# Kernel tuning notes

Hardware: AMD Instinct MI355X
Metric: run time of the kernel (lower is better)

Reference implementation:

```python
import jax, jax.numpy as jnp
import numpy as np

N, E, D = 10000, 160000, 512
H, C = 4, 128          # hidden layers: 4 heads x 128 = 512 (residual-compatible)
HF, CF = 2, 512        # final layer: 2 heads, concat=False (mean)
NEG_SLOPE = 0.2


def _gat(x, src, dst, W, a_src, a_dst, b, heads, out_c, concat):
    """PyG-style GATConv (v1 attention), no dropout (eval mode)."""
    n = x.shape[0]
    h = (x @ W).reshape(n, heads, out_c)                  # [N,H,C]
    es = (h * a_src).sum(-1)                              # [N,H]
    ed = (h * a_dst).sum(-1)                              # [N,H]
    e = jax.nn.leaky_relu(es[src] + ed[dst], NEG_SLOPE)   # [E,H]
    m = jax.ops.segment_max(e, dst, num_segments=n)       # softmax over in-edges of dst
    m = jnp.where(jnp.isfinite(m), m, 0.0)                # guard isolated nodes
    ex = jnp.exp(e - m[dst])
    den = jax.ops.segment_sum(ex, dst, num_segments=n)
    alpha = ex / (den[dst] + 1e-16)                       # [E,H]
    msg = h[src] * alpha[..., None]                       # [E,H,C]
    out = jax.ops.segment_sum(msg, dst, num_segments=n)   # [N,H,C]
    out = out.reshape(n, heads * out_c) if concat else out.mean(axis=1)
    return out + b


def setup_inputs() -> dict:
    key = jax.random.key(0)
    ks = jax.random.split(key, 16)
    s = 0.05
    return {
        "graph": jax.random.normal(ks[0], (N, D), jnp.float32),
        "edge_index": jax.random.randint(ks[1], (2, E), 0, N, dtype=jnp.int32),
        "W1": jax.random.normal(ks[2], (D, H * C), jnp.float32) * s,
        "as1": jax.random.normal(ks[3], (H, C), jnp.float32) * s,
        "ad1": jax.random.normal(ks[4], (H, C), jnp.float32) * s,
        "b1": jnp.zeros((H * C,), jnp.float32),
        "W2": jax.random.normal(ks[5], (H * C, H * C), jnp.float32) * s,
        "as2": jax.random.normal(ks[6], (H, C), jnp.float32) * s,
        "ad2": jax.random.normal(ks[7], (H, C), jnp.float32) * s,
        "b2": jnp.zeros((H * C,), jnp.float32),
        "W3": jax.random.normal(ks[8], (H * C, HF * CF), jnp.float32) * s,
        "as3": jax.random.normal(ks[9], (HF, CF), jnp.float32) * s,
        "ad3": jax.random.normal(ks[10], (HF, CF), jnp.float32) * s,
        "b3": jnp.zeros((CF,), jnp.float32),
    }


def reference(graph, edge_index, W1, as1, ad1, b1, W2, as2, ad2, b2, W3, as3, ad3, b3):
    src, dst = edge_index[0], edge_index[1]
    # layer_size=2: conv1 + convs[0] with ELU+residual, convs[1] (concat=False) residual only
    x = jax.nn.elu(_gat(graph, src, dst, W1, as1, ad1, b1, H, C, True) + graph)
    x = jax.nn.elu(_gat(x, src, dst, W2, as2, ad2, b2, H, C, True) + x)
    x = _gat(x, src, dst, W3, as3, ad3, b3, HF, CF, False) + x
    return x
```

## Files before the change

### kernel.cpp

```cpp
#include <hip/hip_runtime.h>
#include <hip/hip_bf16.h>
#include <hip/hip_fp16.h>
#include <cstddef>
#include <cstdint>


typedef _Float16 half8 __attribute__((ext_vector_type(8)));
typedef _Float16 half4v __attribute__((ext_vector_type(4)));
typedef float floatx4 __attribute__((ext_vector_type(4)));

#define AS1(p) ((const __attribute__((address_space(1))) void*)(p))
#define AS3(p) ((__attribute__((address_space(3))) void*)(p))


__global__ void count_deg(const int* __restrict__ dst, int* __restrict__ deg, int E) {
    int e = blockIdx.x * blockDim.x + threadIdx.x;
    if (e < E) atomicAdd(&deg[dst[e]], 1);
}

__global__ void scan_kernel(const int* __restrict__ deg, int* __restrict__ row_start,
                            int* __restrict__ cursor, int n) {
    __shared__ int wsum[16];
    __shared__ int carry_s;
    int tid = threadIdx.x;
    int wave = tid >> 6, lane = tid & 63;
    if (tid == 0) { carry_s = 0; row_start[0] = 0; }
    __syncthreads();
    for (int base = 0; base < n; base += 1024) {
        int i = base + tid;
        int v = (i < n) ? deg[i] : 0;
        int x = v;
#pragma unroll
        for (int off = 1; off < 64; off <<= 1) {
            int t = __shfl_up(x, off);
            if (lane >= off) x += t;
        }
        if (lane == 63) wsum[wave] = x;
        __syncthreads();
        if (wave == 0 && lane < 16) {
            int w = wsum[lane];
#pragma unroll
            for (int off = 1; off < 16; off <<= 1) {
                int t = __shfl_up(w, off);
                if (lane >= off) w += t;
            }
            wsum[lane] = w;
        }
        __syncthreads();
        int carry = carry_s;
        int incl = x + (wave ? wsum[wave - 1] : 0) + carry;
        if (i < n) { row_start[i + 1] = incl; cursor[i] = incl - v; }
        __syncthreads();
        if (tid == 1023) carry_s = incl;
        __syncthreads();
    }
}

__global__ void scatter_edges(const int* __restrict__ src, const int* __restrict__ dst,
                              int* __restrict__ cursor, int* __restrict__ srcs, int E) {
    int e = blockIdx.x * blockDim.x + threadIdx.x;
    if (e < E) {
        int p = atomicAdd(&cursor[dst[e]], 1);
        srcs[p] = src[e];
    }
}


__global__ void cast_f16(const float* __restrict__ in, _Float16* __restrict__ out, int n4) {
    int i = blockIdx.x * blockDim.x + threadIdx.x;
    if (i < n4) {
        float4 v = ((const float4*)in)[i];
        half4v o = {(_Float16)v.x, (_Float16)v.y, (_Float16)v.z, (_Float16)v.w};
        ((half4v*)out)[i] = o;
    }
}

__global__ void prep_weights(const float* __restrict__ W1, const float* __restrict__ W2,
                             const float* __restrict__ W3,
                             _Float16* __restrict__ Wt1, _Float16* __restrict__ Wt2,
                             _Float16* __restrict__ Bt3) {
    __shared__ float t[32][33];
    int b = blockIdx.x;
    int region = b >> 8, idx = b & 255;
    int r0 = (idx >> 4) * 32, c0 = (idx & 15) * 32;
    const float* in;
    _Float16* out;
    int in_ld, out_ld;
    if (region == 0)      { in = W1;       out = Wt1;       in_ld = 512;  out_ld = 512;  }
    else if (region == 1) { in = W2;       out = Wt2;       in_ld = 512;  out_ld = 512;  }
    else if (region == 2) { in = W3;       out = Bt3;       in_ld = 1024; out_ld = 1024; }
    else                  { in = W3 + 512; out = Bt3 + 512; in_ld = 1024; out_ld = 1024; }
    int tx = threadIdx.x, ty = threadIdx.y;
    for (int i = ty; i < 32; i += 8)
        t[i][tx] = in[(size_t)(r0 + i) * in_ld + c0 + tx];
    __syncthreads();
    for (int i = ty; i < 32; i += 8)
        out[(size_t)(c0 + i) * out_ld + r0 + tx] = (_Float16)t[tx][i];
}

__global__ void proj_all(const float* __restrict__ W1, const float* __restrict__ as1,
                         const float* __restrict__ ad1,
                         const float* __restrict__ W2, const float* __restrict__ as2,
                         const float* __restrict__ ad2,
                         const float* __restrict__ W3, const float* __restrict__ as3,
                         const float* __restrict__ ad3,
                         _Float16* __restrict__ Wt1, _Float16* __restrict__ Wt2,
                         float* __restrict__ wes3, float* __restrict__ wed3) {
    int w = (blockIdx.x * blockDim.x + threadIdx.x) >> 6;
    int lane = threadIdx.x & 63;
    if (w < 8192) {
        int layer = w >> 12;
        int idx = w & 4095;
        int d = idx & 511, hh = (idx >> 9) & 3, sel = idx >> 11;
        const float* W = layer ? W2 : W1;
        const float* a = layer ? (sel ? ad2 : as2) : (sel ? ad1 : as1);
        const float* row = W + (size_t)d * 512 + hh * 128;
        const float* av = a + hh * 128;
        float s = 0.f;
        s += row[lane] * av[lane];
        s += row[lane + 64] * av[lane + 64];
#pragma unroll
        for (int off = 32; off; off >>= 1) s += __shfl_down(s, off);
        if (lane == 0) {
            _Float16* Wt = layer ? Wt2 : Wt1;
            Wt[(size_t)(512 + sel * 4 + hh) * 512 + d] = (_Float16)s;
        }
    } else if (w < 10240) {
        int idx = w - 8192;
        int k = idx & 511, hh = (idx >> 9) & 1, sel = idx >> 10;
        const float* a = (sel ? ad3 : as3) + hh * 512;
        const float* row = W3 + (size_t)k * 1024 + hh * 512;
        float s = 0.f;
        for (int c = lane; c < 512; c += 64) s += row[c] * a[c];
#pragma unroll
        for (int off = 32; off; off >>= 1) s += __shfl_down(s, off);
        if (lane == 0) (sel ? wed3 : wes3)[hh * 512 + k] = s;
    } else if (w < 11136) {
        int z = (w - 10240) * 64 + lane;
        int layer = z / 28672;
        int rem = z - layer * 28672;
        int row = 520 + rem / 512, col = rem & 511;
        (layer ? Wt2 : Wt1)[(size_t)row * 512 + col] = (_Float16)0.f;
    }
}


#define BK 64

__global__ __launch_bounds__(256) void gemm_f16_att(const _Float16* __restrict__ A,
                                                    const _Float16* __restrict__ Bt,
                                                    _Float16* __restrict__ Hout,
                                                    float* __restrict__ es,
                                                    float* __restrict__ ed,
                                                    int M, int K) {
    __shared__ _Float16 As[64 * BK];
    __shared__ _Float16 Bs[64 * BK];
    int tid = threadIdx.x;
    int lane = tid & 63, wave = tid >> 6;
    int wm = (wave & 1) * 32, wn = (wave >> 1) * 32;
    int m0 = blockIdx.y * 64, n0 = blockIdx.x * 64;
    int l15 = lane & 15, quad = lane >> 4;
    int trow = tid >> 3, tcol = tid & 7;

    floatx4 acc[2][2];
#pragma unroll
    for (int i = 0; i < 2; ++i)
#pragma unroll
        for (int j = 0; j < 2; ++j) acc[i][j] = (floatx4){0.f, 0.f, 0.f, 0.f};

    for (int k0 = 0; k0 < K; k0 += BK) {
        __syncthreads();
#pragma unroll
        for (int i = 0; i < 2; ++i) {
            int gr = m0 + i * 32 + trow; if (gr >= M) gr = M - 1;
            __builtin_amdgcn_global_load_lds(AS1(A + (size_t)gr * K + k0 + tcol * 8),
                                             AS3(As + (size_t)(i * 256 + tid) * 8), 16, 0, 0);
        }
#pragma unroll
        for (int i = 0; i < 2; ++i) {
            int gr = n0 + i * 32 + trow;
            __builtin_amdgcn_global_load_lds(AS1(Bt + (size_t)gr * K + k0 + tcol * 8),
                                             AS3(Bs + (size_t)(i * 256 + tid) * 8), 16, 0, 0);
        }
        __syncthreads();
#pragma unroll
        for (int ks = 0; ks < BK; ks += 32) {
            half8 af[2], bfr[2];
#pragma unroll
            for (int i = 0; i < 2; ++i)
                af[i] = *(const half8*)&As[(wm + i * 16 + l15) * BK + ks + quad * 8];
#pragma unroll
            for (int j = 0; j < 2; ++j)
                bfr[j] = *(const half8*)&Bs[(wn + j * 16 + l15) * BK + ks + quad * 8];
#pragma unroll
            for (int i = 0; i < 2; ++i)
#pragma unroll
                for (int j = 0; j < 2; ++j)
                    acc[i][j] = __builtin_amdgcn_mfma_f32_16x16x32_f16(af[i], bfr[j], acc[i][j], 0, 0, 0);
        }
    }
#pragma unroll
    for (int i = 0; i < 2; ++i)
#pragma unroll
        for (int j = 0; j < 2; ++j) {
            int col = n0 + wn + j * 16 + l15;
#pragma unroll
            for (int r = 0; r < 4; ++r) {
                int row = m0 + wm + i * 16 + quad * 4 + r;
                if (row < M) {
                    float v = acc[i][j][r];
                    if (col < 512) Hout[(size_t)row * 512 + col] = (_Float16)v;
                    else if (col < 516) es[row * 4 + col - 512] = v;
                    else if (col < 520) ed[row * 4 + col - 516] = v;
                }
            }
        }
}

__global__ __launch_bounds__(256) void gemm_f16_ep(const _Float16* __restrict__ A,
                                                   const _Float16* __restrict__ Bt,
                                                   float* __restrict__ out,
                                                   const float* __restrict__ bias,
                                                   const _Float16* __restrict__ xres,
                                                   int M, int Nn, int K) {
    __shared__ _Float16 As[64 * BK];
    __shared__ _Float16 Bs[64 * BK];
    int tid = threadIdx.x;
    int lane = tid & 63, wave = tid >> 6;
    int wm = (wave & 1) * 32, wn = (wave >> 1) * 32;
    int m0 = blockIdx.y * 64, n0 = blockIdx.x * 64;
    int l15 = lane & 15, quad = lane >> 4;
    int trow = tid >> 3, tcol = tid & 7;

    floatx4 acc[2][2];
#pragma unroll
    for (int i = 0; i < 2; ++i)
#pragma unroll
        for (int j = 0; j < 2; ++j) acc[i][j] = (floatx4){0.f, 0.f, 0.f, 0.f};

    for (int k0 = 0; k0 < K; k0 += BK) {
        __syncthreads();
#pragma unroll
        for (int i = 0; i < 2; ++i) {
            int gr = m0 + i * 32 + trow; if (gr >= M) gr = M - 1;
            __builtin_amdgcn_global_load_lds(AS1(A + (size_t)gr * K + k0 + tcol * 8),
                                             AS3(As + (size_t)(i * 256 + tid) * 8), 16, 0, 0);
        }
#pragma unroll
        for (int i = 0; i < 2; ++i) {
            int gr = n0 + i * 32 + trow;
            __builtin_amdgcn_global_load_lds(AS1(Bt + (size_t)gr * K + k0 + tcol * 8),
                                             AS3(Bs + (size_t)(i * 256 + tid) * 8), 16, 0, 0);
        }
        __syncthreads();
#pragma unroll
        for (int ks = 0; ks < BK; ks += 32) {
            half8 af[2], bfr[2];
#pragma unroll
            for (int i = 0; i < 2; ++i)
                af[i] = *(const half8*)&As[(wm + i * 16 + l15) * BK + ks + quad * 8];
#pragma unroll
            for (int j = 0; j < 2; ++j)
                bfr[j] = *(const half8*)&Bs[(wn + j * 16 + l15) * BK + ks + quad * 8];
#pragma unroll
            for (int i = 0; i < 2; ++i)
#pragma unroll
                for (int j = 0; j < 2; ++j)
                    acc[i][j] = __builtin_amdgcn_mfma_f32_16x16x32_f16(af[i], bfr[j], acc[i][j], 0, 0, 0);
        }
    }
#pragma unroll
    for (int i = 0; i < 2; ++i)
#pragma unroll
        for (int j = 0; j < 2; ++j) {
            int col = n0 + wn + j * 16 + l15;
#pragma unroll
            for (int r = 0; r < 4; ++r) {
                int row = m0 + wm + i * 16 + quad * 4 + r;
                if (row < M)
                    out[(size_t)row * Nn + col] =
                        0.5f * acc[i][j][r] + bias[col] + (float)xres[(size_t)row * Nn + col];
            }
        }
}


template <int H>
__global__ __launch_bounds__(256) void attn_alpha1(
    const float* __restrict__ es, const float* __restrict__ ed,
    const int* __restrict__ row_start, const int* __restrict__ srcs,
    float* __restrict__ alpha, float* __restrict__ den, int Nn, int E) {
    const int EP = 64 / H;
    int wave = threadIdx.x >> 6, lane = threadIdx.x & 63;
    int n = blockIdx.x * 4 + wave;
    if (n >= Nn) return;
    int h = lane & (H - 1);
    int eslot = lane / H;
    float edn = ed[n * H + h];
    int beg = row_start[n], end = row_start[n + 1];
    float dsum = 0.f;
    for (int j0 = beg; j0 < end; j0 += EP) {
        int j = j0 + eslot;
        if (j < end) {
            float e = es[srcs[j] * H + h] + edn;
            e = (e > 0.f) ? e : 0.2f * e;
            float w = __expf(e);
            alpha[(size_t)h * E + j] = w;
            dsum += w;
        }
    }
#pragma unroll
    for (int off = H; off < 64; off <<= 1) dsum += __shfl_xor(dsum, off);
    if (lane < H) den[n * H + lane] = dsum;
}


template <bool RES32, bool COEF3>
__global__ __launch_bounds__(512) void aggregate6_concat(
    const _Float16* __restrict__ h, const float* __restrict__ alpha,
    const float* __restrict__ den,
    const int* __restrict__ row_start, const int* __restrict__ srcs,
    const float* __restrict__ bias, const float* __restrict__ xres32,
    const _Float16* __restrict__ xres16, _Float16* __restrict__ x_out_h,
    const float* __restrict__ wes3, const float* __restrict__ wed3,
    float* __restrict__ es3, float* __restrict__ ed3, int Nn, int E) {
    int wave = threadIdx.x >> 6, lane = threadIdx.x & 63;
    int n = blockIdx.x * 8 + wave;
    if (n >= Nn) return;
    int head = lane >> 4;
    int c0 = lane * 8;
    const float* al = alpha + (size_t)head * E;
    int beg = row_start[n], end = row_start[n + 1];
    float acc[8] = {};
    int j = beg;
    for (; j + 3 < end; j += 4) {
        int s0 = srcs[j], s1 = srcs[j + 1], s2 = srcs[j + 2], s3 = srcs[j + 3];
        float w0 = al[j], w1 = al[j + 1], w2 = al[j + 2], w3 = al[j + 3];
        half8 h0 = *(const half8*)&h[(size_t)s0 * 512 + c0];
        half8 h1 = *(const half8*)&h[(size_t)s1 * 512 + c0];
        half8 h2 = *(const half8*)&h[(size_t)s2 * 512 + c0];
        half8 h3 = *(const half8*)&h[(size_t)s3 * 512 + c0];
#pragma unroll
        for (int k = 0; k < 8; ++k) acc[k] += w0 * (float)h0[k];
#pragma unroll
        for (int k = 0; k < 8; ++k) acc[k] += w1 * (float)h1[k];
#pragma unroll
        for (int k = 0; k < 8; ++k) acc[k] += w2 * (float)h2[k];
#pragma unroll
        for (int k = 0; k < 8; ++k) acc[k] += w3 * (float)h3[k];
    }
    for (; j < end; ++j) {
        int s = srcs[j];
        float w = al[j];
        half8 hv = *(const half8*)&h[(size_t)s * 512 + c0];
#pragma unroll
        for (int k = 0; k < 8; ++k) acc[k] += w * (float)hv[k];
    }
    float invden = 1.f / (den[n * 4 + head] + 1e-16f);
    size_t base = (size_t)n * 512 + c0;
    float v[8];
    half8 o;
#pragma unroll
    for (int k = 0; k < 8; ++k) {
        float res = RES32 ? xres32[base + k] : (float)xres16[base + k];
        float t = acc[k] * invden + bias[c0 + k] + res;
        t = (t > 0.f) ? t : expm1f(t);
        v[k] = t;
        o[k] = (_Float16)t;
    }
    *(half8*)&x_out_h[base] = o;
    if (COEF3) {
        float t0 = 0.f, t1 = 0.f, t2 = 0.f, t3 = 0.f;
#pragma unroll
        for (int k = 0; k < 8; ++k) {
            t0 += v[k] * wes3[c0 + k];
            t1 += v[k] * wes3[512 + c0 + k];
            t2 += v[k] * wed3[c0 + k];
            t3 += v[k] * wed3[512 + c0 + k];
        }
#pragma unroll
        for (int off = 32; off; off >>= 1) {
            t0 += __shfl_down(t0, off);
            t1 += __shfl_down(t1, off);
            t2 += __shfl_down(t2, off);
            t3 += __shfl_down(t3, off);
        }
        if (lane == 0) {
            es3[n * 2] = t0; es3[n * 2 + 1] = t1;
            ed3[n * 2] = t2; ed3[n * 2 + 1] = t3;
        }
    }
}


__global__ __launch_bounds__(512) void aggregate6_dual(
    const _Float16* __restrict__ x, const float* __restrict__ alpha,
    const float* __restrict__ den,
    const int* __restrict__ row_start, const int* __restrict__ srcs,
    _Float16* __restrict__ y, int Nn, int E) {
    int wave = threadIdx.x >> 6, lane = threadIdx.x & 63;
    int n = blockIdx.x * 8 + wave;
    if (n >= Nn) return;
    int c0 = lane * 8;
    const float* al0 = alpha;
    const float* al1 = alpha + E;
    int beg = row_start[n], end = row_start[n + 1];
    float a0[8] = {}, a1[8] = {};
    int j = beg;
    for (; j + 3 < end; j += 4) {
        int s0 = srcs[j], s1 = srcs[j + 1], s2 = srcs[j + 2], s3 = srcs[j + 3];
        float u0 = al0[j], u1 = al0[j + 1], u2 = al0[j + 2], u3 = al0[j + 3];
        float v0 = al1[j], v1 = al1[j + 1], v2 = al1[j + 2], v3 = al1[j + 3];
        half8 h0 = *(const half8*)&x[(size_t)s0 * 512 + c0];
        half8 h1 = *(const half8*)&x[(size_t)s1 * 512 + c0];
        half8 h2 = *(const half8*)&x[(size_t)s2 * 512 + c0];
        half8 h3 = *(const half8*)&x[(size_t)s3 * 512 + c0];
#pragma unroll
        for (int k = 0; k < 8; ++k) { float f = (float)h0[k]; a0[k] += u0 * f; a1[k] += v0 * f; }
#pragma unroll
        for (int k = 0; k < 8; ++k) { float f = (float)h1[k]; a0[k] += u1 * f; a1[k] += v1 * f; }
#pragma unroll
        for (int k = 0; k < 8; ++k) { float f = (float)h2[k]; a0[k] += u2 * f; a1[k] += v2 * f; }
#pragma unroll
        for (int k = 0; k < 8; ++k) { float f = (float)h3[k]; a0[k] += u3 * f; a1[k] += v3 * f; }
    }
    for (; j < end; ++j) {
        int s = srcs[j];
        float u = al0[j], v = al1[j];
        half8 hv = *(const half8*)&x[(size_t)s * 512 + c0];
#pragma unroll
        for (int k = 0; k < 8; ++k) { float f = (float)hv[k]; a0[k] += u * f; a1[k] += v * f; }
    }
    float invd0 = 1.f / (den[n * 2] + 1e-16f);
    float invd1 = 1.f / (den[n * 2 + 1] + 1e-16f);
    half8 o0, o1;
#pragma unroll
    for (int k = 0; k < 8; ++k) {
        o0[k] = (_Float16)(a0[k] * invd0);
        o1[k] = (_Float16)(a1[k] * invd1);
    }
    *(half8*)&y[(size_t)n * 1024 + c0] = o0;
    *(half8*)&y[(size_t)n * 1024 + 512 + c0] = o1;
}


extern "C" void kernel_launch(void* const* d_in, const int* in_sizes, int n_in,
                              void* d_out, int out_size, void* d_ws, size_t ws_size,
                              hipStream_t stream) {
    const float* graph = (const float*)d_in[0];
    const int* edge_index = (const int*)d_in[1];
    const float* W1 = (const float*)d_in[2];
    const float* as1 = (const float*)d_in[3];
    const float* ad1 = (const float*)d_in[4];
    const float* b1 = (const float*)d_in[5];
    const float* W2 = (const float*)d_in[6];
    const float* as2 = (const float*)d_in[7];
    const float* ad2 = (const float*)d_in[8];
    const float* b2 = (const float*)d_in[9];
    const float* W3 = (const float*)d_in[10];
    const float* as3 = (const float*)d_in[11];
    const float* ad3 = (const float*)d_in[12];
    const float* b3 = (const float*)d_in[13];

    const int D = 512;
    int N = in_sizes[0] / D;
    int E = in_sizes[1] / 2;
    const int* src = edge_index;
    const int* dst = edge_index + E;

    char* p = (char*)d_ws;
    auto carve = [&](size_t bytes) {
        void* r = (void*)p;
        p += (bytes + 255) & ~(size_t)255;
        return r;
    };
    _Float16* Ah   = (_Float16*)carve((size_t)N * 512 * 2);
    _Float16* Wt1  = (_Float16*)carve((size_t)576 * 512 * 2);
    _Float16* Wt2  = (_Float16*)carve((size_t)576 * 512 * 2);
    _Float16* Bt3  = (_Float16*)carve((size_t)512 * 1024 * 2);
    _Float16* h_h  = (_Float16*)carve((size_t)N * 1024 * 2);
    float* es      = (float*)carve((size_t)N * 4 * 4);
    float* ed      = (float*)carve((size_t)N * 4 * 4);
    float* den     = (float*)carve((size_t)N * 4 * 4);
    float* alpha   = (float*)carve((size_t)4 * E * 4);
    float* wes3    = (float*)carve((size_t)2 * 512 * 4);
    float* wed3    = (float*)carve((size_t)2 * 512 * 4);
    int* deg       = (int*)carve((size_t)N * 4);
    int* cur       = (int*)carve((size_t)N * 4);
    int* row_st    = (int*)carve((size_t)(N + 1) * 4);
    int* srcs      = (int*)carve((size_t)E * 4);

    hipMemsetAsync(deg, 0, (size_t)N * 4, stream);
    count_deg<<<(E + 255) / 256, 256, 0, stream>>>(dst, deg, E);
    scan_kernel<<<1, 1024, 0, stream>>>(deg, row_st, cur, N);
    scatter_edges<<<(E + 255) / 256, 256, 0, stream>>>(src, dst, cur, srcs, E);

    cast_f16<<<(N * 512 / 4 + 255) / 256, 256, 0, stream>>>(graph, Ah, N * 512 / 4);
    prep_weights<<<1024, dim3(32, 8), 0, stream>>>(W1, W2, W3, Wt1, Wt2, Bt3);
    proj_all<<<2784, 256, 0, stream>>>(W1, as1, ad1, W2, as2, ad2, W3, as3, ad3,
                                       Wt1, Wt2, wes3, wed3);

    int nblk4 = (N + 3) / 4;
    int nblk8 = (N + 7) / 8;
    int mblk = (N + 63) / 64;
    gemm_f16_att<<<dim3(9, mblk), 256, 0, stream>>>(Ah, Wt1, h_h, es, ed, N, 512);
    attn_alpha1<4><<<nblk4, 256, 0, stream>>>(es, ed, row_st, srcs, alpha, den, N, E);
    aggregate6_concat<true, false><<<nblk8, 512, 0, stream>>>(
        h_h, alpha, den, row_st, srcs, b1, graph, nullptr, Ah,
        nullptr, nullptr, nullptr, nullptr, N, E);

    gemm_f16_att<<<dim3(9, mblk), 256, 0, stream>>>(Ah, Wt2, h_h, es, ed, N, 512);
    attn_alpha1<4><<<nblk4, 256, 0, stream>>>(es, ed, row_st, srcs, alpha, den, N, E);
    aggregate6_concat<false, true><<<nblk8, 512, 0, stream>>>(
        h_h, alpha, den, row_st, srcs, b2, nullptr, Ah, Ah,
        wes3, wed3, es, ed, N, E);

    attn_alpha1<2><<<nblk4, 256, 0, stream>>>(es, ed, row_st, srcs, alpha, den, N, E);
    aggregate6_dual<<<nblk8, 512, 0, stream>>>(Ah, alpha, den, row_st, srcs, h_h, N, E);
    gemm_f16_ep<<<dim3(8, mblk), 256, 0, stream>>>(
        h_h, Bt3, (float*)d_out, b3, Ah, N, 512, 1024);
}
```

Baseline: 323.2 us.

## Fuse attention softmax weight computation into aggregation kernels

Drops the separate attn_alpha1 kernels and the alpha/den buffers, and computes the exp(leaky_relu(es[src]+ed[dst])) edge weights and their per-node sums inside the aggregation loops. This removes three kernel launches and the round trip of writing and re-reading a 4*E alpha array. In exchange, each lane recomputes its head's edge weight (redundant exp across the 16 lanes sharing a head) and does an extra gather of es per edge. Layer-3 coefficients now go to separate es3/ed3 buffers instead of overwriting es/ed.

```diff
diff --git a/kernel.cpp b/kernel.cpp
--- a/kernel.cpp
+++ b/kernel.cpp
@@ -11,6 +11,11 @@
 
 #define AS1(p) ((const __attribute__((address_space(1))) void*)(p))
 #define AS3(p) ((__attribute__((address_space(3))) void*)(p))
+
+__device__ __forceinline__ float leaky_exp(float e) {
+    e = (e > 0.f) ? e : 0.2f * e;
+    return __expf(e);
+}
 
 
 __global__ void count_deg(const int* __restrict__ dst, int* __restrict__ deg, int E) {
@@ -285,61 +290,36 @@
 }
 
 
-template <int H>
-__global__ __launch_bounds__(256) void attn_alpha1(
-    const float* __restrict__ es, const float* __restrict__ ed,
-    const int* __restrict__ row_start, const int* __restrict__ srcs,
-    float* __restrict__ alpha, float* __restrict__ den, int Nn, int E) {
-    const int EP = 64 / H;
-    int wave = threadIdx.x >> 6, lane = threadIdx.x & 63;
-    int n = blockIdx.x * 4 + wave;
-    if (n >= Nn) return;
-    int h = lane & (H - 1);
-    int eslot = lane / H;
-    float edn = ed[n * H + h];
-    int beg = row_start[n], end = row_start[n + 1];
-    float dsum = 0.f;
-    for (int j0 = beg; j0 < end; j0 += EP) {
-        int j = j0 + eslot;
-        if (j < end) {
-            float e = es[srcs[j] * H + h] + edn;
-            e = (e > 0.f) ? e : 0.2f * e;
-            float w = __expf(e);
-            alpha[(size_t)h * E + j] = w;
-            dsum += w;
-        }
-    }
-#pragma unroll
-    for (int off = H; off < 64; off <<= 1) dsum += __shfl_xor(dsum, off);
-    if (lane < H) den[n * H + lane] = dsum;
-}
-
-
 template <bool RES32, bool COEF3>
-__global__ __launch_bounds__(512) void aggregate6_concat(
-    const _Float16* __restrict__ h, const float* __restrict__ alpha,
-    const float* __restrict__ den,
+__global__ __launch_bounds__(512) void aggregate7_concat(
+    const _Float16* __restrict__ h, const float* __restrict__ es,
+    const float* __restrict__ ed,
     const int* __restrict__ row_start, const int* __restrict__ srcs,
     const float* __restrict__ bias, const float* __restrict__ xres32,
     const _Float16* __restrict__ xres16, _Float16* __restrict__ x_out_h,
     const float* __restrict__ wes3, const float* __restrict__ wed3,
-    float* __restrict__ es3, float* __restrict__ ed3, int Nn, int E) {
+    float* __restrict__ es3, float* __restrict__ ed3, int Nn) {
     int wave = threadIdx.x >> 6, lane = threadIdx.x & 63;
     int n = blockIdx.x * 8 + wave;
     if (n >= Nn) return;
     int head = lane >> 4;
     int c0 = lane * 8;
-    const float* al = alpha + (size_t)head * E;
+    float edn = ed[n * 4 + head];
     int beg = row_start[n], end = row_start[n + 1];
     float acc[8] = {};
+    float den = 0.f;
     int j = beg;
     for (; j + 3 < end; j += 4) {
         int s0 = srcs[j], s1 = srcs[j + 1], s2 = srcs[j + 2], s3 = srcs[j + 3];
-        float w0 = al[j], w1 = al[j + 1], w2 = al[j + 2], w3 = al[j + 3];
+        float e0 = es[s0 * 4 + head], e1 = es[s1 * 4 + head];
+        float e2 = es[s2 * 4 + head], e3 = es[s3 * 4 + head];
         half8 h0 = *(const half8*)&h[(size_t)s0 * 512 + c0];
         half8 h1 = *(const half8*)&h[(size_t)s1 * 512 + c0];
         half8 h2 = *(const half8*)&h[(size_t)s2 * 512 + c0];
         half8 h3 = *(const half8*)&h[(size_t)s3 * 512 + c0];
+        float w0 = leaky_exp(e0 + edn), w1 = leaky_exp(e1 + edn);
+        float w2 = leaky_exp(e2 + edn), w3 = leaky_exp(e3 + edn);
+        den += w0 + w1 + w2 + w3;
 #pragma unroll
         for (int k = 0; k < 8; ++k) acc[k] += w0 * (float)h0[k];
 #pragma unroll
@@ -351,12 +331,13 @@
     }
     for (; j < end; ++j) {
         int s = srcs[j];
-        float w = al[j];
+        float w = leaky_exp(es[s * 4 + head] + edn);
         half8 hv = *(const half8*)&h[(size_t)s * 512 + c0];
+        den += w;
 #pragma unroll
         for (int k = 0; k < 8; ++k) acc[k] += w * (float)hv[k];
     }
-    float invden = 1.f / (den[n * 4 + head] + 1e-16f);
+    float invden = 1.f / (den + 1e-16f);
     size_t base = (size_t)n * 512 + c0;
     float v[8];
     half8 o;
@@ -393,28 +374,36 @@
 }
 
 
-__global__ __launch_bounds__(512) void aggregate6_dual(
-    const _Float16* __restrict__ x, const float* __restrict__ alpha,
-    const float* __restrict__ den,
+__global__ __launch_bounds__(512) void aggregate7_dual(
+    const _Float16* __restrict__ x, const float* __restrict__ es3,
+    const float* __restrict__ ed3,
     const int* __restrict__ row_start, const int* __restrict__ srcs,
-    _Float16* __restrict__ y, int Nn, int E) {
+    _Float16* __restrict__ y, int Nn) {
     int wave = threadIdx.x >> 6, lane = threadIdx.x & 63;
     int n = blockIdx.x * 8 + wave;
     if (n >= Nn) return;
     int c0 = lane * 8;
-    const float* al0 = alpha;
-    const float* al1 = alpha + E;
+    float edn0 = ed3[n * 2], edn1 = ed3[n * 2 + 1];
     int beg = row_start[n], end = row_start[n + 1];
     float a0[8] = {}, a1[8] = {};
+    float den0 = 0.f, den1 = 0.f;
     int j = beg;
     for (; j + 3 < end; j += 4) {
         int s0 = srcs[j], s1 = srcs[j + 1], s2 = srcs[j + 2], s3 = srcs[j + 3];
-        float u0 = al0[j], u1 = al0[j + 1], u2 = al0[j + 2], u3 = al0[j + 3];
-        float v0 = al1[j], v1 = al1[j + 1], v2 = al1[j + 2], v3 = al1[j + 3];
+        float2 q0 = *(const float2*)&es3[s0 * 2];
+        float2 q1 = *(const float2*)&es3[s1 * 2];
+        float2 q2 = *(const float2*)&es3[s2 * 2];
+        float2 q3 = *(const float2*)&es3[s3 * 2];
         half8 h0 = *(const half8*)&x[(size_t)s0 * 512 + c0];
         half8 h1 = *(const half8*)&x[(size_t)s1 * 512 + c0];
         half8 h2 = *(const half8*)&x[(size_t)s2 * 512 + c0];
         half8 h3 = *(const half8*)&x[(size_t)s3 * 512 + c0];
+        float u0 = leaky_exp(q0.x + edn0), v0 = leaky_exp(q0.y + edn1);
+        float u1 = leaky_exp(q1.x + edn0), v1 = leaky_exp(q1.y + edn1);
+        float u2 = leaky_exp(q2.x + edn0), v2 = leaky_exp(q2.y + edn1);
+        float u3 = leaky_exp(q3.x + edn0), v3 = leaky_exp(q3.y + edn1);
+        den0 += u0 + u1 + u2 + u3;
+        den1 += v0 + v1 + v2 + v3;
 #pragma unroll
         for (int k = 0; k < 8; ++k) { float f = (float)h0[k]; a0[k] += u0 * f; a1[k] += v0 * f; }
 #pragma unroll
@@ -426,13 +415,15 @@
     }
     for (; j < end; ++j) {
         int s = srcs[j];
-        float u = al0[j], v = al1[j];
+        float2 q = *(const float2*)&es3[s * 2];
+        float u = leaky_exp(q.x + edn0), v = leaky_exp(q.y + edn1);
         half8 hv = *(const half8*)&x[(size_t)s * 512 + c0];
+        den0 += u; den1 += v;
 #pragma unroll
         for (int k = 0; k < 8; ++k) { float f = (float)hv[k]; a0[k] += u * f; a1[k] += v * f; }
     }
-    float invd0 = 1.f / (den[n * 2] + 1e-16f);
-    float invd1 = 1.f / (den[n * 2 + 1] + 1e-16f);
+    float invd0 = 1.f / (den0 + 1e-16f);
+    float invd1 = 1.f / (den1 + 1e-16f);
     half8 o0, o1;
 #pragma unroll
     for (int k = 0; k < 8; ++k) {
@@ -481,8 +472,8 @@
     _Float16* h_h  = (_Float16*)carve((size_t)N * 1024 * 2);
     float* es      = (float*)carve((size_t)N * 4 * 4);
     float* ed      = (float*)carve((size_t)N * 4 * 4);
-    float* den     = (float*)carve((size_t)N * 4 * 4);
-    float* alpha   = (float*)carve((size_t)4 * E * 4);
+    float* es3     = (float*)carve((size_t)N * 2 * 4);
+    float* ed3     = (float*)carve((size_t)N * 2 * 4);
     float* wes3    = (float*)carve((size_t)2 * 512 * 4);
     float* wed3    = (float*)carve((size_t)2 * 512 * 4);
     int* deg       = (int*)carve((size_t)N * 4);
@@ -500,23 +491,19 @@
     proj_all<<<2784, 256, 0, stream>>>(W1, as1, ad1, W2, as2, ad2, W3, as3, ad3,
                                        Wt1, Wt2, wes3, wed3);
 
-    int nblk4 = (N + 3) / 4;
     int nblk8 = (N + 7) / 8;
     int mblk = (N + 63) / 64;
     gemm_f16_att<<<dim3(9, mblk), 256, 0, stream>>>(Ah, Wt1, h_h, es, ed, N, 512);
-    attn_alpha1<4><<<nblk4, 256, 0, stream>>>(es, ed, row_st, srcs, alpha, den, N, E);
-    aggregate6_concat<true, false><<<nblk8, 512, 0, stream>>>(
-        h_h, alpha, den, row_st, srcs, b1, graph, nullptr, Ah,
-        nullptr, nullptr, nullptr, nullptr, N, E);
+    aggregate7_concat<true, false><<<nblk8, 512, 0, stream>>>(
+        h_h, es, ed, row_st, srcs, b1, graph, nullptr, Ah,
+        nullptr, nullptr, nullptr, nullptr, N);
 
     gemm_f16_att<<<dim3(9, mblk), 256, 0, stream>>>(Ah, Wt2, h_h, es, ed, N, 512);
-    attn_alpha1<4><<<nblk4, 256, 0, stream>>>(es, ed, row_st, srcs, alpha, den, N, E);
-    aggregate6_concat<false, true><<<nblk8, 512, 0, stream>>>(
-        h_h, alpha, den, row_st, srcs, b2, nullptr, Ah, Ah,
-        wes3, wed3, es, ed, N, E);
-
-    attn_alpha1<2><<<nblk4, 256, 0, stream>>>(es, ed, row_st, srcs, alpha, den, N, E);
-    aggregate6_dual<<<nblk8, 512, 0, stream>>>(Ah, alpha, den, row_st, srcs, h_h, N, E);
+    aggregate7_concat<false, true><<<nblk8, 512, 0, stream>>>(
+        h_h, es, ed, row_st, srcs, b2, nullptr, Ah, Ah,
+        wes3, wed3, es3, ed3, N);
+
+    aggregate7_dual<<<nblk8, 512, 0, stream>>>(Ah, es3, ed3, row_st, srcs, h_h, N);
     gemm_f16_ep<<<dim3(8, mblk), 256, 0, stream>>>(
         h_h, Bt3, (float*)d_out, b3, Ah, N, 512, 1024);
 }
```

After: 311.2 us. -3.7%, faster.
